# Kernel tuning notes

Hardware: AMD Instinct MI355X
Metric: run time of the kernel (lower is better)

Reference implementation:

```python
import jax, jax.numpy as jnp
import numpy as np

B, S, D = 2, 2048, 2048
H, KVH, HD = 16, 4, 128
I = 8192
EPS = 1e-6
SCALE = HD ** -0.5
NEG = -1e9


def rms_norm(x, w):
    xf = x.astype(jnp.float32)
    var = jnp.mean(xf * xf, axis=-1, keepdims=True)
    return (w * (xf * jax.lax.rsqrt(var + EPS)).astype(x.dtype))


def rope(x, cos_f, sin_f):
    # x: (B, h, S, HD); cos_f/sin_f: (B, 1, S, HD//2). Interleaved pairs.
    xp = x.reshape(*x.shape[:-1], HD // 2, 2)
    xr, xi = xp[..., 0], xp[..., 1]
    rr = cos_f * xr - sin_f * xi
    ri = sin_f * xr + cos_f * xi
    return jnp.stack([rr, ri], axis=-1).reshape(x.shape)


def setup_inputs() -> dict:
    key = jax.random.key(0)
    ks = jax.random.split(key, 12)
    inp = {
        "hidden_states": jax.random.normal(ks[0], (B, S, D), jnp.float32),
        "cos": jax.random.normal(ks[1], (B, S, HD), jnp.float32),
        "sin": jax.random.normal(ks[2], (B, S, HD), jnp.float32),
    }
    # additive causal mask (B,1,S,S)
    causal = jnp.tril(jnp.ones((S, S), jnp.bool_))
    inp["attention_mask"] = jnp.where(causal, 0.0, NEG).astype(jnp.float32)[None, None].repeat(B, 0)
    sc = 0.02
    inp["wq"] = jax.random.normal(ks[3], (H * HD, D), jnp.float32) * sc
    inp["wk"] = jax.random.normal(ks[4], (KVH * HD, D), jnp.float32) * sc
    inp["wv"] = jax.random.normal(ks[5], (KVH * HD, D), jnp.float32) * sc
    inp["wo"] = jax.random.normal(ks[6], (D, H * HD), jnp.float32) * sc
    inp["w_gate"] = jax.random.normal(ks[7], (I, D), jnp.float32) * sc
    inp["w_up"] = jax.random.normal(ks[8], (I, D), jnp.float32) * sc
    inp["w_down"] = jax.random.normal(ks[9], (D, I), jnp.float32) * sc
    inp["ln1_w"] = jnp.ones((D,), jnp.float32)
    inp["ln2_w"] = jnp.ones((D,), jnp.float32)
    return inp


def layer_fwd(hidden_states, cos, sin, attention_mask,
              wq, wk, wv, wo, w_gate, w_up, w_down, ln1_w, ln2_w):
    residual = hidden_states
    h = rms_norm(hidden_states, ln1_w)
    # projections
    q = jnp.einsum('bsd,ed->bse', h, wq).reshape(B, S, H, HD).transpose(0, 2, 1, 3)
    k = jnp.einsum('bsd,ed->bse', h, wk).reshape(B, S, KVH, HD).transpose(0, 2, 1, 3)
    v = jnp.einsum('bsd,ed->bse', h, wv).reshape(B, S, KVH, HD).transpose(0, 2, 1, 3)
    cos_f = cos[..., :HD // 2][:, None]  # (B,1,S,HD/2)
    sin_f = sin[..., :HD // 2][:, None]
    q = rope(q, cos_f, sin_f)
    k = rope(k, cos_f, sin_f)
    # GQA: repeat_interleave kv heads
    n_rep = H // KVH
    k = jnp.repeat(k, n_rep, axis=1)
    v = jnp.repeat(v, n_rep, axis=1)
    scores = jnp.einsum('bhqd,bhkd->bhqk', q, k) * SCALE + attention_mask
    probs = jax.nn.softmax(scores.astype(jnp.float32), axis=-1).astype(q.dtype)
    attn = jnp.einsum('bhqk,bhkd->bhqd', probs, v)
    attn = attn.transpose(0, 2, 1, 3).reshape(B, S, H * HD)
    attn_out = jnp.einsum('bse,de->bsd', attn, wo)
    h = residual + attn_out
    residual = h
    m = rms_norm(h, ln2_w)
    gate = jax.nn.silu(jnp.einsum('bsd,id->bsi', m, w_gate))
    up = jnp.einsum('bsd,id->bsi', m, w_up)
    mlp_out = jnp.einsum('bsi,di->bsd', gate * up, w_down)
    return residual + mlp_out


def reference(hidden_states, cos, sin, attention_mask,
              wq, wk, wv, wo, w_gate, w_up, w_down, ln1_w, ln2_w):
    return layer_fwd(hidden_states, cos, sin, attention_mask,
                     wq, wk, wv, wo, w_gate, w_up, w_down, ln1_w, ln2_w)
```

## Files before the change

### kernel.cpp

```cpp
#include <hip/hip_runtime.h>
#include <cstdint>
#include <cstddef>

typedef unsigned short u16;
typedef short bf16x8 __attribute__((ext_vector_type(8)));
typedef float floatx4 __attribute__((ext_vector_type(4)));

__device__ __forceinline__ float b2f(u16 u) {
    union { unsigned int i; float f; } v; v.i = ((unsigned int)u) << 16; return v.f;
}
__device__ __forceinline__ u16 f2b(float f) {
    union { float f; unsigned int i; } v; v.f = f;
    unsigned int u = v.i;
    unsigned int r = (u + 0x7fffu + ((u >> 16) & 1u)) >> 16;
    return (u16)r;
}

#define GLL16(gptr, lptr)                                                          \
    __builtin_amdgcn_global_load_lds(                                              \
        (__attribute__((address_space(1))) void*)(gptr),                           \
        (__attribute__((address_space(3))) void*)(lptr), 16, 0, 0)

#define BAR_LGKM() asm volatile("s_waitcnt lgkmcnt(0)\n\ts_barrier" ::: "memory")
#define WAIT_VM8_BAR() asm volatile("s_waitcnt vmcnt(8)\n\ts_barrier" ::: "memory")
#define WAIT_VM0_BAR() asm volatile("s_waitcnt vmcnt(0)\n\ts_barrier" ::: "memory")

__global__ __launch_bounds__(256) void cvt_all(
    const float* __restrict__ wq, const float* __restrict__ wk,
    const float* __restrict__ wvp, const float* __restrict__ wo,
    const float* __restrict__ wg, const float* __restrict__ wu,
    const float* __restrict__ wd,
    u16* __restrict__ wqkv, u16* __restrict__ wob, u16* __restrict__ wgb,
    u16* __restrict__ wub, u16* __restrict__ wdb) {
    long v = (long)blockIdx.x * 256 + threadIdx.x;
    const float* s; u16* d; long o;
    if (v < 1048576)       { s = wq;  d = wqkv;           o = v; }
    else if (v < 1310720)  { s = wk;  d = wqkv + 4194304; o = v - 1048576; }
    else if (v < 1572864)  { s = wvp; d = wqkv + 5242880; o = v - 1310720; }
    else if (v < 2621440)  { s = wo;  d = wob;            o = v - 1572864; }
    else if (v < 6815744)  { s = wg;  d = wgb;            o = v - 2621440; }
    else if (v < 11010048) { s = wu;  d = wub;            o = v - 6815744; }
    else                   { s = wd;  d = wdb;            o = v - 11010048; }
    float4 x = ((const float4*)s)[o];
    u16 t[4] = { f2b(x.x), f2b(x.y), f2b(x.z), f2b(x.w) };
    ((ushort4*)d)[o] = *(const ushort4*)t;
}

__global__ __launch_bounds__(256) void rmsnorm_kernel(const float* __restrict__ x,
                                                      const float* __restrict__ w,
                                                      u16* __restrict__ out) {
    __shared__ float red[4];
    const int row = blockIdx.x;
    const float* xr = x + (size_t)row * 2048;
    const int d0 = threadIdx.x * 8;
    float4 a = *(const float4*)&xr[d0];
    float4 b = *(const float4*)&xr[d0 + 4];
    float s = a.x*a.x + a.y*a.y + a.z*a.z + a.w*a.w +
              b.x*b.x + b.y*b.y + b.z*b.z + b.w*b.w;
    #pragma unroll
    for (int m = 1; m < 64; m <<= 1) s += __shfl_xor(s, m);
    const int lane = threadIdx.x & 63, wv = threadIdx.x >> 6;
    if (lane == 0) red[wv] = s;
    __syncthreads();
    float tot = red[0] + red[1] + red[2] + red[3];
    float r = rsqrtf(tot * (1.0f / 2048.0f) + 1e-6f);
    const float* wp = w + d0;
    u16 o[8];
    o[0] = f2b(a.x * r * wp[0]); o[1] = f2b(a.y * r * wp[1]);
    o[2] = f2b(a.z * r * wp[2]); o[3] = f2b(a.w * r * wp[3]);
    o[4] = f2b(b.x * r * wp[4]); o[5] = f2b(b.y * r * wp[5]);
    o[6] = f2b(b.z * r * wp[6]); o[7] = f2b(b.w * r * wp[7]);
    *(bf16x8*)&out[(size_t)row * 2048 + d0] = *(const bf16x8*)o;
}

__global__ __launch_bounds__(256, 2) void gemm_bt(
    const u16* __restrict__ A, const u16* __restrict__ W,
    int M, int N, int K, int mode,
    u16* __restrict__ outb, float* __restrict__ outf,
    const float* __restrict__ res) {

    __shared__ __align__(16) u16 smA[2][128 * 64];
    __shared__ __align__(16) u16 smB[2][128 * 64];

    const int tid  = threadIdx.x;
    const int lane = tid & 63;
    const int c    = lane & 15;
    const int quad = lane >> 4;
    const int wv   = tid >> 6;
    const int wm   = (wv >> 1) * 64;
    const int wn   = (wv & 1) * 64;
    const int row0 = blockIdx.y * 128;
    const int col0 = blockIdx.x * 128;

    const u16* aB[4]; const u16* bB[4]; int lo[4];
    #pragma unroll
    for (int p = 0; p < 4; ++p) {
        int lin = p * 256 + tid, r = lin >> 3, g = lin & 7, sg = g ^ (r & 7);
        aB[p] = A + (size_t)(row0 + r) * K + sg * 8;
        bB[p] = W + (size_t)(col0 + r) * K + sg * 8;
        lo[p] = lin * 8;
    }
    #pragma unroll
    for (int p = 0; p < 4; ++p) { GLL16(aB[p], &smA[0][lo[p]]); GLL16(bB[p], &smB[0][lo[p]]); }

    floatx4 acc[4][4] = {};
    const int nk = K >> 6;
    for (int k = 0; k < nk; ++k) {
        BAR_LGKM();
        if (k + 1 < nk) {
            const int nb = (k + 1) & 1, ko = (k + 1) << 6;
            #pragma unroll
            for (int p = 0; p < 4; ++p) {
                GLL16(aB[p] + ko, &smA[nb][lo[p]]);
                GLL16(bB[p] + ko, &smB[nb][lo[p]]);
            }
            WAIT_VM8_BAR();
        } else {
            WAIT_VM0_BAR();
        }
        const u16* sA = smA[k & 1];
        const u16* sB = smB[k & 1];
        #pragma unroll
        for (int ks = 0; ks < 2; ++ks) {
            bf16x8 af[4], bfr[4];
            #pragma unroll
            for (int mi = 0; mi < 4; ++mi) {
                int r = wm + mi * 16 + c;
                int pos = (ks * 4 + quad) ^ (c & 7);
                af[mi] = *(const bf16x8*)&sA[r * 64 + pos * 8];
            }
            #pragma unroll
            for (int ni = 0; ni < 4; ++ni) {
                int r = wn + ni * 16 + c;
                int pos = (ks * 4 + quad) ^ (c & 7);
                bfr[ni] = *(const bf16x8*)&sB[r * 64 + pos * 8];
            }
            #pragma unroll
            for (int mi = 0; mi < 4; ++mi)
                #pragma unroll
                for (int ni = 0; ni < 4; ++ni)
                    acc[mi][ni] = __builtin_amdgcn_mfma_f32_16x16x32_bf16(
                        af[mi], bfr[ni], acc[mi][ni], 0, 0, 0);
        }
    }

    #pragma unroll
    for (int mi = 0; mi < 4; ++mi) {
        #pragma unroll
        for (int r = 0; r < 4; ++r) {
            int row = row0 + wm + mi * 16 + quad * 4 + r;
            #pragma unroll
            for (int ni = 0; ni < 4; ++ni) {
                int col = col0 + wn + ni * 16 + c;
                size_t idx = (size_t)row * N + col;
                float v = acc[mi][ni][r];
                if (mode == 0) outb[idx] = f2b(v);
                else           outf[idx] = v + res[idx];
            }
        }
    }
}

__global__ __launch_bounds__(256, 2) void mlp_gateup(
    const u16* __restrict__ A, const u16* __restrict__ Wg,
    const u16* __restrict__ Wu, u16* __restrict__ out) {

    __shared__ __align__(16) u16 smA[2][128 * 64];
    __shared__ __align__(16) u16 smG[2][64 * 64];
    __shared__ __align__(16) u16 smU[2][64 * 64];

    const int K = 2048;
    const int tid  = threadIdx.x;
    const int lane = tid & 63;
    const int c    = lane & 15;
    const int quad = lane >> 4;
    const int wv   = tid >> 6;
    const int wm   = wv * 32;
    const int row0 = blockIdx.y * 128;
    const int col0 = blockIdx.x * 64;

    const u16* aB[4]; int loA[4];
    #pragma unroll
    for (int p = 0; p < 4; ++p) {
        int lin = p * 256 + tid, r = lin >> 3, g = lin & 7, sg = g ^ (r & 7);
        aB[p] = A + (size_t)(row0 + r) * K + sg * 8;
        loA[p] = lin * 8;
    }
    const u16* gB[2]; const u16* uB[2]; int loGU[2];
    #pragma unroll
    for (int p = 0; p < 2; ++p) {
        int lin = p * 256 + tid, r = lin >> 3, g = lin & 7, sg = g ^ (r & 7);
        gB[p] = Wg + (size_t)(col0 + r) * K + sg * 8;
        uB[p] = Wu + (size_t)(col0 + r) * K + sg * 8;
        loGU[p] = lin * 8;
    }
    #pragma unroll
    for (int p = 0; p < 4; ++p) GLL16(aB[p], &smA[0][loA[p]]);
    #pragma unroll
    for (int p = 0; p < 2; ++p) { GLL16(gB[p], &smG[0][loGU[p]]); GLL16(uB[p], &smU[0][loGU[p]]); }

    floatx4 ag[2][4] = {}, au[2][4] = {};
    const int nk = K >> 6;
    for (int k = 0; k < nk; ++k) {
        BAR_LGKM();
        if (k + 1 < nk) {
            const int nb = (k + 1) & 1, ko = (k + 1) << 6;
            #pragma unroll
            for (int p = 0; p < 4; ++p) GLL16(aB[p] + ko, &smA[nb][loA[p]]);
            #pragma unroll
            for (int p = 0; p < 2; ++p) {
                GLL16(gB[p] + ko, &smG[nb][loGU[p]]);
                GLL16(uB[p] + ko, &smU[nb][loGU[p]]);
            }
            WAIT_VM8_BAR();
        } else {
            WAIT_VM0_BAR();
        }
        const u16* sA = smA[k & 1];
        const u16* sG = smG[k & 1];
        const u16* sU = smU[k & 1];
        #pragma unroll
        for (int ks = 0; ks < 2; ++ks) {
            int pos;
            bf16x8 af[2], bg[4], bu[4];
            #pragma unroll
            for (int mi = 0; mi < 2; ++mi) {
                int r = wm + mi * 16 + c;
                pos = (ks * 4 + quad) ^ (c & 7);
                af[mi] = *(const bf16x8*)&sA[r * 64 + pos * 8];
            }
            #pragma unroll
            for (int ni = 0; ni < 4; ++ni) {
                int r = ni * 16 + c;
                pos = (ks * 4 + quad) ^ (c & 7);
                bg[ni] = *(const bf16x8*)&sG[r * 64 + pos * 8];
                bu[ni] = *(const bf16x8*)&sU[r * 64 + pos * 8];
            }
            #pragma unroll
            for (int mi = 0; mi < 2; ++mi)
                #pragma unroll
                for (int ni = 0; ni < 4; ++ni) {
                    ag[mi][ni] = __builtin_amdgcn_mfma_f32_16x16x32_bf16(
                        af[mi], bg[ni], ag[mi][ni], 0, 0, 0);
                    au[mi][ni] = __builtin_amdgcn_mfma_f32_16x16x32_bf16(
                        af[mi], bu[ni], au[mi][ni], 0, 0, 0);
                }
        }
    }

    #pragma unroll
    for (int mi = 0; mi < 2; ++mi) {
        #pragma unroll
        for (int r = 0; r < 4; ++r) {
            int row = row0 + wm + mi * 16 + quad * 4 + r;
            #pragma unroll
            for (int ni = 0; ni < 4; ++ni) {
                int col = col0 + ni * 16 + c;
                float g = ag[mi][ni][r];
                float u = au[mi][ni][r];
                float sg_ = g / (1.0f + __expf(-g));
                out[(size_t)row * 8192 + col] = f2b(sg_ * u);
            }
        }
    }
}

__global__ __launch_bounds__(256) void rope_kernel(u16* __restrict__ qkv,
                                                   const float* __restrict__ cs,
                                                   const float* __restrict__ sn) {
    const int t = blockIdx.x;
    const int hh = blockIdx.y * 4 + (threadIdx.x >> 6);
    const int j = threadIdx.x & 63;
    size_t base = (size_t)t * 3072 + (hh < 16 ? hh * 128 : 2048 + (hh - 16) * 128);
    float cf = cs[(size_t)t * 128 + j];
    float sf = sn[(size_t)t * 128 + j];
    ushort2 xv = *(ushort2*)&qkv[base + 2 * j];
    float xr = b2f(xv.x), xi = b2f(xv.y);
    ushort2 ov;
    ov.x = f2b(cf * xr - sf * xi);
    ov.y = f2b(sf * xr + cf * xi);
    *(ushort2*)&qkv[base + 2 * j] = ov;
}

__global__ __launch_bounds__(256) void transpose_v(const u16* __restrict__ qkv,
                                                   u16* __restrict__ vt) {
    __shared__ __align__(16) u16 T[64][136];
    const int bkv = blockIdx.x;
    const int st = blockIdx.y;
    const int b = bkv >> 2, kvh = bkv & 3;
    const int tid = threadIdx.x;
    #pragma unroll
    for (int it = 0; it < 4; ++it) {
        int lin = it * 256 + tid;
        int sr = lin >> 4, gr = lin & 15;
        bf16x8 v = *(const bf16x8*)&qkv[((size_t)(b * 2048 + st * 64 + sr)) * 3072 +
                                        2560 + kvh * 128 + gr * 8];
        *(bf16x8*)&T[sr][gr * 8] = v;
    }
    __syncthreads();
    #pragma unroll
    for (int it = 0; it < 4; ++it) {
        int lin = it * 256 + tid;
        int n = lin >> 3, sc = lin & 7;
        u16 tmp[8];
        #pragma unroll
        for (int j = 0; j < 8; ++j) tmp[j] = T[sc * 8 + j][n];
        *(bf16x8*)&vt[((size_t)(bkv * 128 + n)) * 2048 + st * 64 + sc * 8] =
            *(const bf16x8*)tmp;
    }
}

__global__ __launch_bounds__(256, 2) void attn_kernel(const u16* __restrict__ qkv,
                                                      const u16* __restrict__ vt,
                                                      u16* __restrict__ attnb) {
    __shared__ __align__(16) u16 sK[64 * 128];
    __shared__ __align__(16) u16 sV[128 * 64];
    __shared__ __align__(16) u16 sP[4][16 * 80];

    const int tid  = threadIdx.x;
    const int lane = tid & 63;
    const int c    = lane & 15;
    const int quad = lane >> 4;
    const int wv   = tid >> 6;

    const int qt  = 31 - (int)blockIdx.x;
    const int bh  = blockIdx.y;
    const int b   = bh >> 4;
    const int h   = bh & 15;
    const int kvh = h >> 2;

    const int qrow = qt * 64 + wv * 16 + c;
    const size_t qbase = ((size_t)(b * 2048 + qrow)) * 3072 + h * 128;
    bf16x8 qf[4];
    #pragma unroll
    for (int kk = 0; kk < 4; ++kk)
        qf[kk] = *(const bf16x8*)&qkv[qbase + kk * 32 + quad * 8];

    floatx4 o[8] = {};
    float m_[4], l_[4];
    #pragma unroll
    for (int r = 0; r < 4; ++r) { m_[r] = -__builtin_inff(); l_[r] = 0.0f; }

    const float SC = 0.08838834764831845f;

    for (int kt = 0; kt <= qt; ++kt) {
        const int kv0 = kt * 64;
        __syncthreads();
        #pragma unroll
        for (int p = 0; p < 4; ++p) {
            int lin = p * 256 + tid;
            {
                int r = lin >> 4, g = lin & 15;
                int sg = g ^ (r & 7);
                const u16* gk = qkv + ((size_t)(b * 2048 + kv0 + r)) * 3072 +
                                2048 + kvh * 128 + sg * 8;
                GLL16(gk, &sK[lin * 8]);
            }
            {
                int r = lin >> 3, g = lin & 7;
                int sg = g ^ (r & 7);
                const u16* gv = vt + ((size_t)((b * 4 + kvh) * 128 + r)) * 2048 +
                                kv0 + sg * 8;
                GLL16(gv, &sV[lin * 8]);
            }
        }
        __syncthreads();

        floatx4 s[4] = {};
        #pragma unroll
        for (int kk = 0; kk < 4; ++kk) {
            #pragma unroll
            for (int ct = 0; ct < 4; ++ct) {
                int rk = ct * 16 + c;
                int pos = (kk * 4 + quad) ^ (c & 7);
                bf16x8 kf = *(const bf16x8*)&sK[rk * 128 + pos * 8];
                s[ct] = __builtin_amdgcn_mfma_f32_16x16x32_bf16(qf[kk], kf, s[ct], 0, 0, 0);
            }
        }

        const int qloc = wv * 16 + quad * 4;
        #pragma unroll
        for (int ct = 0; ct < 4; ++ct) {
            #pragma unroll
            for (int r = 0; r < 4; ++r) {
                float v = s[ct][r] * SC;
                if (kt == qt && (ct * 16 + c) > (qloc + r)) v = -__builtin_inff();
                s[ct][r] = v;
            }
        }

        float alpha[4];
        #pragma unroll
        for (int r = 0; r < 4; ++r) {
            float rm = fmaxf(fmaxf(s[0][r], s[1][r]), fmaxf(s[2][r], s[3][r]));
            rm = fmaxf(rm, __shfl_xor(rm, 1));
            rm = fmaxf(rm, __shfl_xor(rm, 2));
            rm = fmaxf(rm, __shfl_xor(rm, 4));
            rm = fmaxf(rm, __shfl_xor(rm, 8));
            float mn = fmaxf(m_[r], rm);
            alpha[r] = __expf(m_[r] - mn);
            m_[r] = mn;
        }
        #pragma unroll
        for (int r = 0; r < 4; ++r) {
            float rs = 0.0f;
            #pragma unroll
            for (int ct = 0; ct < 4; ++ct) {
                float p = __expf(s[ct][r] - m_[r]);
                s[ct][r] = p;
                rs += p;
            }
            rs += __shfl_xor(rs, 1);
            rs += __shfl_xor(rs, 2);
            rs += __shfl_xor(rs, 4);
            rs += __shfl_xor(rs, 8);
            l_[r] = l_[r] * alpha[r] + rs;
        }

        u16* sp = &sP[wv][0];
        #pragma unroll
        for (int ct = 0; ct < 4; ++ct)
            #pragma unroll
            for (int r = 0; r < 4; ++r)
                sp[(quad * 4 + r) * 80 + ct * 16 + c] = f2b(s[ct][r]);

        #pragma unroll
        for (int nt = 0; nt < 8; ++nt)
            #pragma unroll
            for (int r = 0; r < 4; ++r)
                o[nt][r] *= alpha[r];

        #pragma unroll
        for (int ks2 = 0; ks2 < 2; ++ks2) {
            bf16x8 pa = *(const bf16x8*)&sp[c * 80 + ks2 * 32 + quad * 8];
            #pragma unroll
            for (int nt = 0; nt < 8; ++nt) {
                int rv = nt * 16 + c;
                int pos = (ks2 * 4 + quad) ^ (c & 7);
                bf16x8 vb = *(const bf16x8*)&sV[rv * 64 + pos * 8];
                o[nt] = __builtin_amdgcn_mfma_f32_16x16x32_bf16(pa, vb, o[nt], 0, 0, 0);
            }
        }
    }

    float inv[4];
    #pragma unroll
    for (int r = 0; r < 4; ++r) inv[r] = 1.0f / l_[r];
    #pragma unroll
    for (int nt = 0; nt < 8; ++nt) {
        #pragma unroll
        for (int r = 0; r < 4; ++r) {
            int row = qt * 64 + wv * 16 + quad * 4 + r;
            int col = h * 128 + nt * 16 + c;
            attnb[((size_t)(b * 2048 + row)) * 2048 + col] = f2b(o[nt][r] * inv[r]);
        }
    }
}

extern "C" void kernel_launch(void* const* d_in, const int* in_sizes, int n_in,
                              void* d_out, int out_size, void* d_ws, size_t ws_size,
                              hipStream_t stream) {
    const float* hidden = (const float*)d_in[0];
    const float* cosp   = (const float*)d_in[1];
    const float* sinp   = (const float*)d_in[2];
    const float* wq  = (const float*)d_in[4];
    const float* wk  = (const float*)d_in[5];
    const float* wvp = (const float*)d_in[6];
    const float* wo  = (const float*)d_in[7];
    const float* wg  = (const float*)d_in[8];
    const float* wu  = (const float*)d_in[9];
    const float* wd  = (const float*)d_in[10];
    const float* ln1 = (const float*)d_in[11];
    const float* ln2 = (const float*)d_in[12];
    float* outp = (float*)d_out;

    char* ws = (char*)d_ws;
    size_t off = 0;
    auto alloc = [&](size_t bytes) {
        void* p = ws + off;
        off += (bytes + 255) & ~(size_t)255;
        return p;
    };
    u16* wqkv_b  = (u16*)alloc((size_t)3072 * 2048 * 2);
    u16* wo_b    = (u16*)alloc((size_t)2048 * 2048 * 2);
    u16* wg_b    = (u16*)alloc((size_t)8192 * 2048 * 2);
    u16* wu_b    = (u16*)alloc((size_t)8192 * 2048 * 2);
    u16* wd_b    = (u16*)alloc((size_t)2048 * 8192 * 2);
    u16* normed  = (u16*)alloc((size_t)4096 * 2048 * 2);
    u16* qkv     = (u16*)alloc((size_t)4096 * 3072 * 2);
    u16* vtb     = (u16*)alloc((size_t)8 * 128 * 2048 * 2);
    u16* attnb   = (u16*)alloc((size_t)4096 * 2048 * 2);
    float* h1    = (float*)alloc((size_t)4096 * 2048 * 4);
    u16* hidprod = (u16*)alloc((size_t)4096 * 8192 * 2);
    (void)ws_size; (void)in_sizes; (void)n_in; (void)out_size;

    cvt_all<<<59392, 256, 0, stream>>>(wq, wk, wvp, wo, wg, wu, wd,
                                       wqkv_b, wo_b, wg_b, wu_b, wd_b);

    rmsnorm_kernel<<<4096, 256, 0, stream>>>(hidden, ln1, normed);

    gemm_bt<<<dim3(24, 32), 256, 0, stream>>>(normed, wqkv_b, 4096, 3072, 2048, 0,
                                              qkv, nullptr, nullptr);

    rope_kernel<<<dim3(4096, 5), 256, 0, stream>>>(qkv, cosp, sinp);
    transpose_v<<<dim3(8, 32), 256, 0, stream>>>(qkv, vtb);
    attn_kernel<<<dim3(32, 32), 256, 0, stream>>>(qkv, vtb, attnb);

    gemm_bt<<<dim3(16, 32), 256, 0, stream>>>(attnb, wo_b, 4096, 2048, 2048, 1,
                                              nullptr, h1, hidden);

    rmsnorm_kernel<<<4096, 256, 0, stream>>>(h1, ln2, normed);

    mlp_gateup<<<dim3(128, 32), 256, 0, stream>>>(normed, wg_b, wu_b, hidprod);

    gemm_bt<<<dim3(16, 32), 256, 0, stream>>>(hidprod, wd_b, 4096, 2048, 8192, 1,
                                              nullptr, outp, h1);
}
```

Baseline: 1.107 ms.

## Enlarge gate/up MLP tile to 256x128 with 8 waves and phased MFMA scheduling

The fused gate/up SiLU GEMM now uses 512-thread blocks computing a 256x128 output tile instead of 128x64, with waves arranged 2x4 so each wave holds 128x32 of both gate and up accumulators. B fragments are loaded once per k-step and A fragments in four phases, each wrapped in barriers and s_setprio to interleave LDS reads with MFMA bursts across waves. The larger tile raises arithmetic intensity and cuts global/LDS traffic per FLOP. The cost is doubled LDS (about 128KB for the double buffers) and many more accumulator registers, which lowers occupancy. The initial LDS wait barrier was also removed.

```diff
diff --git a/kernel.cpp b/kernel.cpp
--- a/kernel.cpp
+++ b/kernel.cpp
@@ -161,13 +161,13 @@
     }
 }
 
-__global__ __launch_bounds__(256, 2) void mlp_gateup(
+__global__ __launch_bounds__(512, 2) void mlp_gateup2(
     const u16* __restrict__ A, const u16* __restrict__ Wg,
     const u16* __restrict__ Wu, u16* __restrict__ out) {
 
-    __shared__ __align__(16) u16 smA[2][128 * 64];
-    __shared__ __align__(16) u16 smG[2][64 * 64];
-    __shared__ __align__(16) u16 smU[2][64 * 64];
+    __shared__ __align__(16) u16 smA[2][256 * 64];
+    __shared__ __align__(16) u16 smG[2][128 * 64];
+    __shared__ __align__(16) u16 smU[2][128 * 64];
 
     const int K = 2048;
     const int tid  = threadIdx.x;
@@ -175,21 +175,22 @@
     const int c    = lane & 15;
     const int quad = lane >> 4;
     const int wv   = tid >> 6;
-    const int wm   = wv * 32;
-    const int row0 = blockIdx.y * 128;
-    const int col0 = blockIdx.x * 64;
+    const int wm   = (wv >> 2) * 128;
+    const int wn   = (wv & 3) * 32;
+    const int row0 = blockIdx.y * 256;
+    const int col0 = blockIdx.x * 128;
 
     const u16* aB[4]; int loA[4];
     #pragma unroll
     for (int p = 0; p < 4; ++p) {
-        int lin = p * 256 + tid, r = lin >> 3, g = lin & 7, sg = g ^ (r & 7);
+        int lin = p * 512 + tid, r = lin >> 3, g = lin & 7, sg = g ^ (r & 7);
         aB[p] = A + (size_t)(row0 + r) * K + sg * 8;
         loA[p] = lin * 8;
     }
     const u16* gB[2]; const u16* uB[2]; int loGU[2];
     #pragma unroll
     for (int p = 0; p < 2; ++p) {
-        int lin = p * 256 + tid, r = lin >> 3, g = lin & 7, sg = g ^ (r & 7);
+        int lin = p * 512 + tid, r = lin >> 3, g = lin & 7, sg = g ^ (r & 7);
         gB[p] = Wg + (size_t)(col0 + r) * K + sg * 8;
         uB[p] = Wu + (size_t)(col0 + r) * K + sg * 8;
         loGU[p] = lin * 8;
@@ -199,10 +200,9 @@
     #pragma unroll
     for (int p = 0; p < 2; ++p) { GLL16(gB[p], &smG[0][loGU[p]]); GLL16(uB[p], &smU[0][loGU[p]]); }
 
-    floatx4 ag[2][4] = {}, au[2][4] = {};
+    floatx4 ag[8][2] = {}, au[8][2] = {};
     const int nk = K >> 6;
     for (int k = 0; k < nk; ++k) {
-        BAR_LGKM();
         if (k + 1 < nk) {
             const int nb = (k + 1) & 1, ko = (k + 1) << 6;
             #pragma unroll
@@ -219,43 +219,55 @@
         const u16* sA = smA[k & 1];
         const u16* sG = smG[k & 1];
         const u16* sU = smU[k & 1];
-        #pragma unroll
-        for (int ks = 0; ks < 2; ++ks) {
-            int pos;
-            bf16x8 af[2], bg[4], bu[4];
-            #pragma unroll
-            for (int mi = 0; mi < 2; ++mi) {
-                int r = wm + mi * 16 + c;
-                pos = (ks * 4 + quad) ^ (c & 7);
-                af[mi] = *(const bf16x8*)&sA[r * 64 + pos * 8];
-            }
-            #pragma unroll
-            for (int ni = 0; ni < 4; ++ni) {
-                int r = ni * 16 + c;
-                pos = (ks * 4 + quad) ^ (c & 7);
-                bg[ni] = *(const bf16x8*)&sG[r * 64 + pos * 8];
-                bu[ni] = *(const bf16x8*)&sU[r * 64 + pos * 8];
-            }
+
+        bf16x8 bg[2][2], bu[2][2];
+        #pragma unroll
+        for (int ks = 0; ks < 2; ++ks)
+            #pragma unroll
+            for (int ni = 0; ni < 2; ++ni) {
+                int r = wn + ni * 16 + c;
+                int pos = (ks * 4 + quad) ^ (c & 7);
+                bg[ni][ks] = *(const bf16x8*)&sG[r * 64 + pos * 8];
+                bu[ni][ks] = *(const bf16x8*)&sU[r * 64 + pos * 8];
+            }
+
+        #pragma unroll
+        for (int ph = 0; ph < 4; ++ph) {
+            bf16x8 af[2][2];
             #pragma unroll
             for (int mi = 0; mi < 2; ++mi)
                 #pragma unroll
-                for (int ni = 0; ni < 4; ++ni) {
-                    ag[mi][ni] = __builtin_amdgcn_mfma_f32_16x16x32_bf16(
-                        af[mi], bg[ni], ag[mi][ni], 0, 0, 0);
-                    au[mi][ni] = __builtin_amdgcn_mfma_f32_16x16x32_bf16(
-                        af[mi], bu[ni], au[mi][ni], 0, 0, 0);
+                for (int ks = 0; ks < 2; ++ks) {
+                    int r = wm + (ph * 2 + mi) * 16 + c;
+                    int pos = (ks * 4 + quad) ^ (c & 7);
+                    af[mi][ks] = *(const bf16x8*)&sA[r * 64 + pos * 8];
                 }
-        }
-    }
-
-    #pragma unroll
-    for (int mi = 0; mi < 2; ++mi) {
+            __builtin_amdgcn_s_barrier();
+            __builtin_amdgcn_s_setprio(1);
+            #pragma unroll
+            for (int mi = 0; mi < 2; ++mi)
+                #pragma unroll
+                for (int ks = 0; ks < 2; ++ks)
+                    #pragma unroll
+                    for (int ni = 0; ni < 2; ++ni) {
+                        ag[ph * 2 + mi][ni] = __builtin_amdgcn_mfma_f32_16x16x32_bf16(
+                            af[mi][ks], bg[ni][ks], ag[ph * 2 + mi][ni], 0, 0, 0);
+                        au[ph * 2 + mi][ni] = __builtin_amdgcn_mfma_f32_16x16x32_bf16(
+                            af[mi][ks], bu[ni][ks], au[ph * 2 + mi][ni], 0, 0, 0);
+                    }
+            __builtin_amdgcn_s_setprio(0);
+            __builtin_amdgcn_s_barrier();
+        }
+    }
+
+    #pragma unroll
+    for (int mi = 0; mi < 8; ++mi) {
         #pragma unroll
         for (int r = 0; r < 4; ++r) {
             int row = row0 + wm + mi * 16 + quad * 4 + r;
             #pragma unroll
-            for (int ni = 0; ni < 4; ++ni) {
-                int col = col0 + ni * 16 + c;
+            for (int ni = 0; ni < 2; ++ni) {
+                int col = col0 + wn + ni * 16 + c;
                 float g = ag[mi][ni][r];
                 float u = au[mi][ni][r];
                 float sg_ = g / (1.0f + __expf(-g));
@@ -511,7 +523,7 @@
 
     rmsnorm_kernel<<<4096, 256, 0, stream>>>(h1, ln2, normed);
 
-    mlp_gateup<<<dim3(128, 32), 256, 0, stream>>>(normed, wg_b, wu_b, hidprod);
+    mlp_gateup2<<<dim3(64, 16), 512, 0, stream>>>(normed, wg_b, wu_b, hidprod);
 
     gemm_bt<<<dim3(16, 32), 256, 0, stream>>>(hidprod, wd_b, 4096, 2048, 8192, 1,
                                               nullptr, outp, h1);
```

New measurement: 1.115 ms. Within noise of the previous version (+0.8%).
